# Performance work log

Hardware: AMD Instinct MI355X
Metric: run time of the kernel (lower is better)

Reference implementation:

```python
import jax, jax.numpy as jnp
import numpy as np

LN_EPS = 1e-3  # keras LayerNormalization default epsilon


def setup_inputs() -> dict:
    key = jax.random.key(0)
    ks = jax.random.split(key, 6)
    B, H, W, C = 8, 64, 64, 256
    s = 1.0 / np.sqrt(C)
    return {
        "x": jax.random.normal(ks[0], (B, H, W, C), jnp.float32),
        "gamma": jnp.ones((C,), jnp.float32),
        "beta": jnp.zeros((C,), jnp.float32),
        "wq": jax.random.normal(ks[1], (C, C), jnp.float32) * s,
        "bq": jnp.zeros((C,), jnp.float32),
        "wk": jax.random.normal(ks[2], (C, C), jnp.float32) * s,
        "bk": jnp.zeros((C,), jnp.float32),
        "wv": jax.random.normal(ks[3], (C, C), jnp.float32) * s,
        "bv": jnp.zeros((C,), jnp.float32),
        "wo": jax.random.normal(ks[4], (C, C), jnp.float32) * s,
        "bo": jnp.zeros((C,), jnp.float32),
    }


def reference(x, gamma, beta, wq, bq, wk, bk, wv, bv, wo, bo):
    B, H, W, C = x.shape
    # LayerNormalization over channel axis (keras default axis=-1, eps=1e-3)
    mean = jnp.mean(x, axis=-1, keepdims=True)
    var = jnp.mean(jnp.square(x - mean), axis=-1, keepdims=True)
    h = (x - mean) * jax.lax.rsqrt(var + LN_EPS) * gamma + beta

    q = h @ wq + bq
    k = h @ wk + bk
    v = h @ wv + bv

    # flatten spatial dims: single-head attention over N = H*W positions
    N = H * W
    qf = q.reshape(B, N, C)
    kf = k.reshape(B, N, C)
    vf = v.reshape(B, N, C)

    scale = jnp.asarray(C, x.dtype) ** -0.5
    scores = jnp.einsum('bnc,bmc->bnm', qf, kf) * scale  # [B, N, N]
    attn = jax.nn.softmax(scores, axis=-1)
    o = jnp.einsum('bnm,bmc->bnc', attn, vf).reshape(B, H, W, C)

    o = o @ wo + bo
    return x + o
```

## Files before the change

kernel.cpp:

```cpp
#include <hip/hip_runtime.h>
#include <hip/hip_bf16.h>
#include <stdint.h>

typedef __attribute__((ext_vector_type(8))) short bf16x8;
typedef __attribute__((ext_vector_type(4))) short s16x4;
typedef __attribute__((ext_vector_type(4))) float f32x4;

__device__ __forceinline__ unsigned short f2b(float x) {
  __hip_bfloat16 h = __float2bfloat16(x);
  unsigned short u;
  __builtin_memcpy(&u, &h, 2);
  return u;
}

__device__ __forceinline__ float b2f(unsigned short u) {
  unsigned v = (unsigned)u << 16;
  float f;
  __builtin_memcpy(&f, &v, 4);
  return f;
}

__device__ __forceinline__ void glds16(const void* g, void* l) {
  __builtin_amdgcn_global_load_lds((const __attribute__((address_space(1))) void*)g,
                                   (__attribute__((address_space(3))) void*)l,
                                   16, 0, 0);
}

__global__ __launch_bounds__(256) void gemm_qkv(
    const unsigned short* __restrict__ h, const unsigned short* __restrict__ wT,
    const float* __restrict__ bq, const float* __restrict__ bk, const float* __restrict__ bv,
    unsigned short* __restrict__ q, unsigned short* __restrict__ kk,
    unsigned short* __restrict__ vT, float qscale)
{
  __shared__ unsigned short As[128 * 32];
  __shared__ unsigned short Bs[128 * 32];
  const int t = threadIdx.x;
  const int lane = t & 63;
  const int wv_ = t >> 6;
  const int wr = wv_ >> 1, wc = wv_ & 1;
  const int z = blockIdx.z;
  const long long row0 = (long long)blockIdx.y * 128;
  const int col0 = blockIdx.x * 128;
  const unsigned short* Bt = wT + z * 65536;
  const float* bias = z == 0 ? bq : z == 1 ? bk : bv;
  const float scale = z == 0 ? qscale : 1.0f;

  const int sr = t >> 2;
  const int sc = (t & 3) * 8;
  const unsigned short* ga = h + (row0 + sr) * 256 + sc;
  const unsigned short* gb = Bt + (col0 + sr) * 256 + sc;
  char* lA = (char*)As + (t >> 6) * 1024;
  char* lB = (char*)Bs + (t >> 6) * 1024;

  const int l15 = lane & 15;
  const int l4 = lane >> 4;
  const unsigned short* pa = As + (wr * 64 + l15) * 32 + l4 * 8;
  const unsigned short* pb = Bs + (wc * 64 + l15) * 32 + l4 * 8;

  f32x4 acc[4][4] = {};

  for (int k0 = 0; k0 < 256; k0 += 32) {
    glds16(ga, lA);
    glds16(ga + 64 * 256, lA + 4096);
    glds16(gb, lB);
    glds16(gb + 64 * 256, lB + 4096);
    ga += 32;
    gb += 32;
    __syncthreads();
    bf16x8 a[4], b[4];
#pragma unroll
    for (int i = 0; i < 4; i++) a[i] = *(const bf16x8*)(pa + i * 512);
#pragma unroll
    for (int j = 0; j < 4; j++) b[j] = *(const bf16x8*)(pb + j * 512);
#pragma unroll
    for (int i = 0; i < 4; i++)
#pragma unroll
      for (int j = 0; j < 4; j++)
        acc[i][j] = __builtin_amdgcn_mfma_f32_16x16x32_bf16(a[i], b[j], acc[i][j], 0, 0, 0);
    __syncthreads();
  }

#pragma unroll
  for (int i = 0; i < 4; i++) {
#pragma unroll
    for (int j = 0; j < 4; j++) {
      const int col = col0 + wc * 64 + j * 16 + l15;
      const float bv_ = bias[col];
#pragma unroll
      for (int r = 0; r < 4; r++) {
        const long long row = row0 + wr * 64 + i * 16 + l4 * 4 + r;
        const float val = (acc[i][j][r] + bv_) * scale;
        if (z == 0) {
          q[row * 256 + col] = f2b(val);
        } else if (z == 1) {
          kk[row * 256 + col] = f2b(val);
        } else {
          const int bb = (int)(row >> 12), rr = (int)(row & 4095);
          const int kl = rr & 31;
          const int rrp = (rr & ~31) | ((((kl >> 2) & 3) << 3) | (((kl >> 4) & 1) << 2) | (kl & 3));
          vT[((long long)bb * 256 + col) * 4096 + rrp] = f2b(val);
        }
      }
    }
  }
}

__global__ __launch_bounds__(256) void gemm_out(
    const unsigned short* __restrict__ o0, const unsigned short* __restrict__ o1,
    const float2* __restrict__ ml0, const float2* __restrict__ ml1,
    const unsigned short* __restrict__ Bt,
    float* __restrict__ C, const float* __restrict__ bias,
    const float* __restrict__ resid)
{
  __shared__ unsigned short As[128 * 32];
  __shared__ unsigned short Bs[128 * 32];
  const int t = threadIdx.x;
  const int lane = t & 63;
  const int wv_ = t >> 6;
  const int wr = wv_ >> 1, wc = wv_ & 1;
  const long long row0 = (long long)blockIdx.y * 128;
  const int col0 = blockIdx.x * 128;

  const int sr = t >> 2;
  const int sc = (t & 3) * 8;
  const long long ar0 = row0 + sr;
  float f0a, f1a, f0b, f1b;
  {
    const float2 a = ml0[ar0], c = ml1[ar0];
    const float M = fmaxf(a.x, c.x);
    const float w0 = exp2f(a.x - M), w1 = exp2f(c.x - M);
    const float inv = 1.f / (w0 * a.y + w1 * c.y);
    f0a = w0 * inv;
    f1a = w1 * inv;
  }
  {
    const float2 a = ml0[ar0 + 64], c = ml1[ar0 + 64];
    const float M = fmaxf(a.x, c.x);
    const float w0 = exp2f(a.x - M), w1 = exp2f(c.x - M);
    const float inv = 1.f / (w0 * a.y + w1 * c.y);
    f0b = w0 * inv;
    f1b = w1 * inv;
  }
  const unsigned short* g0 = o0 + ar0 * 256 + sc;
  const unsigned short* g1 = o1 + ar0 * 256 + sc;
  const unsigned short* gb = Bt + (col0 + sr) * 256 + sc;
  char* lB = (char*)Bs + (t >> 6) * 1024;

  const int l15 = lane & 15;
  const int l4 = lane >> 4;
  const unsigned short* pa = As + (wr * 64 + l15) * 32 + l4 * 8;
  const unsigned short* pb = Bs + (wc * 64 + l15) * 32 + l4 * 8;

  f32x4 acc[4][4] = {};

  for (int k0 = 0; k0 < 256; k0 += 32) {
    bf16x8 u0 = *(const bf16x8*)g0;
    bf16x8 u1 = *(const bf16x8*)g1;
    bf16x8 v0 = *(const bf16x8*)(g0 + 64 * 256);
    bf16x8 v1 = *(const bf16x8*)(g1 + 64 * 256);
    bf16x8 m0, m1;
#pragma unroll
    for (int e = 0; e < 8; e++) {
      m0[e] = (short)f2b(f0a * b2f((unsigned short)u0[e]) + f1a * b2f((unsigned short)u1[e]));
      m1[e] = (short)f2b(f0b * b2f((unsigned short)v0[e]) + f1b * b2f((unsigned short)v1[e]));
    }
    *(bf16x8*)((char*)As + t * 16) = m0;
    *(bf16x8*)((char*)As + 4096 + t * 16) = m1;
    glds16(gb, lB);
    glds16(gb + 64 * 256, lB + 4096);
    g0 += 32;
    g1 += 32;
    gb += 32;
    __syncthreads();
    bf16x8 a[4], b[4];
#pragma unroll
    for (int i = 0; i < 4; i++) a[i] = *(const bf16x8*)(pa + i * 512);
#pragma unroll
    for (int j = 0; j < 4; j++) b[j] = *(const bf16x8*)(pb + j * 512);
#pragma unroll
    for (int i = 0; i < 4; i++)
#pragma unroll
      for (int j = 0; j < 4; j++)
        acc[i][j] = __builtin_amdgcn_mfma_f32_16x16x32_bf16(a[i], b[j], acc[i][j], 0, 0, 0);
    __syncthreads();
  }

#pragma unroll
  for (int i = 0; i < 4; i++) {
#pragma unroll
    for (int j = 0; j < 4; j++) {
      const int col = col0 + wc * 64 + j * 16 + l15;
      const float bv_ = bias[col];
#pragma unroll
      for (int r = 0; r < 4; r++) {
        const long long row = row0 + wr * 64 + i * 16 + l4 * 4 + r;
        const long long idx = row * 256 + col;
        C[idx] = resid[idx] + acc[i][j][r] + bv_;
      }
    }
  }
}

__global__ __launch_bounds__(512) void ln_bf16(const float* __restrict__ x,
                                               const float* __restrict__ gamma,
                                               const float* __restrict__ beta,
                                               unsigned short* __restrict__ h)
{
  const int w = threadIdx.x >> 6;
  const int lane = threadIdx.x & 63;
  const long long row = (long long)blockIdx.x * 8 + w;
  const f32x4 v = *(const f32x4*)(x + row * 256 + lane * 4);
  const f32x4 g = *(const f32x4*)(gamma + lane * 4);
  const f32x4 be = *(const f32x4*)(beta + lane * 4);
  float s = v[0] + v[1] + v[2] + v[3];
  float s2 = v[0] * v[0] + v[1] * v[1] + v[2] * v[2] + v[3] * v[3];
#pragma unroll
  for (int o = 32; o >= 1; o >>= 1) {
    s += __shfl_xor(s, o, 64);
    s2 += __shfl_xor(s2, o, 64);
  }
  const float mean = s * (1.f / 256.f);
  const float var = s2 * (1.f / 256.f) - mean * mean;
  const float rstd = rsqrtf(var + 1e-3f);
  s16x4 out;
#pragma unroll
  for (int e = 0; e < 4; e++) out[e] = (short)f2b((v[e] - mean) * rstd * g[e] + be[e]);
  *(s16x4*)(h + row * 256 + lane * 4) = out;
}

__global__ void wtrans(const float* __restrict__ wq, const float* __restrict__ wk,
                       const float* __restrict__ wv, const float* __restrict__ wo,
                       unsigned short* __restrict__ wT)
{
  const float* w = blockIdx.z == 0 ? wq : blockIdx.z == 1 ? wk : blockIdx.z == 2 ? wv : wo;
  unsigned short* o = wT + (long long)blockIdx.z * 65536;
  __shared__ float tile[16][17];
  const int tx = threadIdx.x, ty = threadIdx.y;
  const int bx = blockIdx.x * 16, by = blockIdx.y * 16;
  tile[ty][tx] = w[(by + ty) * 256 + bx + tx];
  __syncthreads();
  o[(bx + ty) * 256 + (by + tx)] = f2b(tile[tx][ty]);
}

#define FL_LDS (64 * 1024)

__global__ __launch_bounds__(256, 2) void flash(
    const unsigned short* __restrict__ q,
    const unsigned short* __restrict__ kk,
    const unsigned short* __restrict__ vT,
    unsigned short* __restrict__ o0,
    unsigned short* __restrict__ o1,
    float2* __restrict__ ml0,
    float2* __restrict__ ml1)
{
  extern __shared__ char lds[];
  const int t = threadIdx.x;
  const int w = t >> 6;
  const int lane = t & 63;
  const int l15 = lane & 15, hi = lane >> 4;
  const int b = blockIdx.x & 7;
  const int kh = (blockIdx.x >> 3) & 1;
  const int qb = blockIdx.x >> 4;
  const long long qrow = (long long)b * 4096 + (long long)qb * 128 + w * 32;

  const unsigned short* kbase = kk + (long long)b * 4096 * 256 + (long long)kh * 2048 * 256;
  const unsigned short* vbase = vT + (long long)b * 256 * 4096 + kh * 2048;

  const int gs_k = (t & 31) ^ ((t >> 5) & 7);
  const unsigned short* Kst = kbase + (t >> 5) * 256 + gs_k * 8;
  const int gs_v = (t & 3) ^ ((t >> 2) & 3);
  const unsigned short* Vst = vbase + (long long)(t >> 2) * 4096 + gs_v * 8;

  bf16x8 Qf[2][8];
#pragma unroll
  for (int qg = 0; qg < 2; qg++) {
    const unsigned short* qp = q + (qrow + qg * 16 + l15) * 256 + hi * 8;
#pragma unroll
    for (int ks = 0; ks < 8; ks++) Qf[qg][ks] = *(const bf16x8*)(qp + ks * 32);
  }

  f32x4 O[2][16] = {};
  float mrow[2] = {-1e30f, -1e30f};
  float lrow[2] = {0.f, 0.f};

  auto stage = [&](int it, int c) {
    const unsigned short* ks_ = Kst + (long long)it * 32 * 256;
    const unsigned short* vs_ = Vst + it * 32;
    char* kd = lds + c * 16384 + w * 1024;
    char* vd = lds + 32768 + c * 16384 + w * 1024;
#pragma unroll
    for (int p = 0; p < 4; p++) {
      glds16(ks_ + p * 8 * 256, kd + p * 4096);
      glds16(vs_ + (long long)p * 64 * 4096, vd + p * 4096);
    }
  };

  stage(0, 0);

  for (int it = 0; it < 64; ++it) {
    const int cur = it & 1;
    __builtin_amdgcn_s_barrier();
    if (it < 63) {
      stage(it + 1, cur ^ 1);
      asm volatile("s_waitcnt vmcnt(8)" ::: "memory");
    } else {
      asm volatile("s_waitcnt vmcnt(0)" ::: "memory");
    }
    __builtin_amdgcn_sched_barrier(0);
    __builtin_amdgcn_s_barrier();
    const char* Kb = lds + cur * 16384;
    const char* Vb = lds + 32768 + cur * 16384;

    f32x4 S[2][2] = {};
    __builtin_amdgcn_s_setprio(1);
#pragma unroll
    for (int ks = 0; ks < 8; ks++) {
#pragma unroll
      for (int j = 0; j < 2; j++) {
        bf16x8 Kf = *(const bf16x8*)(Kb + (j * 16 + l15) * 512 +
                                     ((ks * 64 + hi * 16) ^ ((l15 & 7) << 4)));
        S[0][j] = __builtin_amdgcn_mfma_f32_16x16x32_bf16(Kf, Qf[0][ks], S[0][j], 0, 0, 0);
        S[1][j] = __builtin_amdgcn_mfma_f32_16x16x32_bf16(Kf, Qf[1][ks], S[1][j], 0, 0, 0);
      }
    }
    __builtin_amdgcn_s_setprio(0);

    bf16x8 Pf8[2];
#pragma unroll
    for (int qg = 0; qg < 2; qg++) {
      const float mxl =
          fmaxf(fmaxf(fmaxf(S[qg][0][0], S[qg][0][1]), fmaxf(S[qg][0][2], S[qg][0][3])),
                fmaxf(fmaxf(S[qg][1][0], S[qg][1][1]), fmaxf(S[qg][1][2], S[qg][1][3])));
      if (!__all(mxl <= mrow[qg] + 8.f)) {
        float mx = fmaxf(mxl, __shfl_xor(mxl, 16, 64));
        mx = fmaxf(mx, __shfl_xor(mx, 32, 64));
        const float mn = fmaxf(mrow[qg], mx);
        const float rs_ = exp2f(mrow[qg] - mn);
        mrow[qg] = mn;
        lrow[qg] *= rs_;
#pragma unroll
        for (int dg = 0; dg < 16; dg++) O[qg][dg] *= rs_;
      }
      float sum = 0.f;
      float e[2][4];
#pragma unroll
      for (int j = 0; j < 2; j++)
#pragma unroll
        for (int r = 0; r < 4; r++) {
          e[j][r] = exp2f(S[qg][j][r] - mrow[qg]);
          sum += e[j][r];
        }
      lrow[qg] += sum;
      bf16x8 p;
#pragma unroll
      for (int j = 0; j < 2; j++)
#pragma unroll
        for (int r = 0; r < 4; r++) p[j * 4 + r] = (short)f2b(e[j][r]);
      Pf8[qg] = p;
    }

    __builtin_amdgcn_s_setprio(1);
#pragma unroll
    for (int dg = 0; dg < 16; dg++) {
      bf16x8 Vf8 = *(const bf16x8*)(Vb + (dg * 16 + l15) * 64 +
                                    ((hi * 16) ^ ((l15 & 3) << 4)));
      O[0][dg] = __builtin_amdgcn_mfma_f32_16x16x32_bf16(Vf8, Pf8[0], O[0][dg], 0, 0, 0);
      O[1][dg] = __builtin_amdgcn_mfma_f32_16x16x32_bf16(Vf8, Pf8[1], O[1][dg], 0, 0, 0);
    }
    __builtin_amdgcn_s_setprio(0);
  }

  unsigned short* const op = kh ? o1 : o0;
  float2* const mlp = kh ? ml1 : ml0;
  __syncthreads();
  char* const slab = lds + w * 16384;
#pragma unroll
  for (int qg = 0; qg < 2; qg++) {
    float lr = lrow[qg];
    lr += __shfl_xor(lr, 16, 64);
    lr += __shfl_xor(lr, 32, 64);
#pragma unroll
    for (int dg = 0; dg < 16; dg++) {
      f32x4 v = O[qg][dg];
      *(f32x4*)(slab + l15 * 1024 + ((dg * 64 + hi * 16) ^ ((l15 & 7) << 4))) = v;
    }
    if (hi == 0) mlp[qrow + qg * 16 + l15] = make_float2(mrow[qg], lr);
    const int qq = lane >> 2;
    const int dc = lane & 3;
    const long long orow = (qrow + qg * 16 + qq) * 256 + dc * 64;
#pragma unroll
    for (int half = 0; half < 8; half++) {
      bf16x8 pack;
#pragma unroll
      for (int di = 0; di < 2; di++) {
        f32x4 v = *(const f32x4*)(slab + qq * 1024 +
                                  ((dc * 256 + half * 32 + di * 16) ^ ((qq & 7) << 4)));
#pragma unroll
        for (int e2 = 0; e2 < 4; e2++) pack[di * 4 + e2] = (short)f2b(v[e2]);
      }
      *(bf16x8*)(op + orow + half * 8) = pack;
    }
    __syncthreads();
  }
}

extern "C" void kernel_launch(void* const* d_in, const int* in_sizes, int n_in,
                              void* d_out, int out_size, void* d_ws, size_t ws_size,
                              hipStream_t stream)
{
  const float* x = (const float*)d_in[0];
  const float* gamma = (const float*)d_in[1];
  const float* beta = (const float*)d_in[2];
  const float* wq = (const float*)d_in[3];
  const float* bq = (const float*)d_in[4];
  const float* wk = (const float*)d_in[5];
  const float* bk = (const float*)d_in[6];
  const float* wv = (const float*)d_in[7];
  const float* bv = (const float*)d_in[8];
  const float* wo = (const float*)d_in[9];
  const float* bo = (const float*)d_in[10];

  const int Cc = 256;
  const long long MR = 32768;

  char* base = (char*)d_ws;
  size_t off = 0;
  auto take = [&](size_t bytes) -> char* {
    char* p = base + off;
    off = (off + bytes + 255) & ~(size_t)255;
    return p;
  };
  unsigned short* h   = (unsigned short*)take((size_t)MR * Cc * 2);
  unsigned short* q   = (unsigned short*)take((size_t)MR * Cc * 2);
  unsigned short* kk  = (unsigned short*)take((size_t)MR * Cc * 2);
  unsigned short* vT  = (unsigned short*)take((size_t)MR * Cc * 2);
  unsigned short* o0  = (unsigned short*)take((size_t)MR * Cc * 2);
  unsigned short* o1  = (unsigned short*)take((size_t)MR * Cc * 2);
  unsigned short* wT  = (unsigned short*)take(4ull * Cc * Cc * 2);
  float2* ml0 = (float2*)take((size_t)MR * sizeof(float2));
  float2* ml1 = (float2*)take((size_t)MR * sizeof(float2));

  wtrans<<<dim3(16, 16, 4), dim3(16, 16), 0, stream>>>(wq, wk, wv, wo, wT);
  ln_bf16<<<dim3((unsigned)(MR / 8)), dim3(512), 0, stream>>>(x, gamma, beta, h);

  const float qscale = 0.0625f * 1.44269504f;
  gemm_qkv<<<dim3(2, 256, 3), 256, 0, stream>>>(h, wT, bq, bk, bv, q, kk, vT, qscale);

  flash<<<dim3(512), dim3(256), FL_LDS, stream>>>(q, kk, vT, o0, o1, ml0, ml1);

  gemm_out<<<dim3(2, 256, 1), 256, 0, stream>>>(o0, o1, ml0, ml1, wT + 3 * 65536,
                                                (float*)d_out, bo, x);
}
```

Measured before the change: 228.4 us.

## Split flash attention keys three ways and single-buffer K to raise occupancy

```diff
diff --git a/kernel.cpp b/kernel.cpp
--- a/kernel.cpp
+++ b/kernel.cpp
@@ -107,7 +107,9 @@
 
 __global__ __launch_bounds__(256) void gemm_out(
     const unsigned short* __restrict__ o0, const unsigned short* __restrict__ o1,
+    const unsigned short* __restrict__ o2,
     const float2* __restrict__ ml0, const float2* __restrict__ ml1,
+    const float2* __restrict__ ml2,
     const unsigned short* __restrict__ Bt,
     float* __restrict__ C, const float* __restrict__ bias,
     const float* __restrict__ resid)
@@ -124,25 +126,21 @@
   const int sr = t >> 2;
   const int sc = (t & 3) * 8;
   const long long ar0 = row0 + sr;
-  float f0a, f1a, f0b, f1b;
-  {
-    const float2 a = ml0[ar0], c = ml1[ar0];
-    const float M = fmaxf(a.x, c.x);
-    const float w0 = exp2f(a.x - M), w1 = exp2f(c.x - M);
-    const float inv = 1.f / (w0 * a.y + w1 * c.y);
-    f0a = w0 * inv;
-    f1a = w1 * inv;
-  }
-  {
-    const float2 a = ml0[ar0 + 64], c = ml1[ar0 + 64];
-    const float M = fmaxf(a.x, c.x);
-    const float w0 = exp2f(a.x - M), w1 = exp2f(c.x - M);
-    const float inv = 1.f / (w0 * a.y + w1 * c.y);
-    f0b = w0 * inv;
-    f1b = w1 * inv;
+  float fA[2][3];
+#pragma unroll
+  for (int rr = 0; rr < 2; rr++) {
+    const long long row = ar0 + rr * 64;
+    const float2 a = ml0[row], c = ml1[row], d = ml2[row];
+    const float M = fmaxf(fmaxf(a.x, c.x), d.x);
+    const float w0 = exp2f(a.x - M), w1 = exp2f(c.x - M), w2 = exp2f(d.x - M);
+    const float inv = 1.f / (w0 * a.y + w1 * c.y + w2 * d.y);
+    fA[rr][0] = w0 * inv;
+    fA[rr][1] = w1 * inv;
+    fA[rr][2] = w2 * inv;
   }
   const unsigned short* g0 = o0 + ar0 * 256 + sc;
   const unsigned short* g1 = o1 + ar0 * 256 + sc;
+  const unsigned short* g2 = o2 + ar0 * 256 + sc;
   const unsigned short* gb = Bt + (col0 + sr) * 256 + sc;
   char* lB = (char*)Bs + (t >> 6) * 1024;
 
@@ -154,22 +152,24 @@
   f32x4 acc[4][4] = {};
 
   for (int k0 = 0; k0 < 256; k0 += 32) {
-    bf16x8 u0 = *(const bf16x8*)g0;
-    bf16x8 u1 = *(const bf16x8*)g1;
-    bf16x8 v0 = *(const bf16x8*)(g0 + 64 * 256);
-    bf16x8 v1 = *(const bf16x8*)(g1 + 64 * 256);
-    bf16x8 m0, m1;
-#pragma unroll
-    for (int e = 0; e < 8; e++) {
-      m0[e] = (short)f2b(f0a * b2f((unsigned short)u0[e]) + f1a * b2f((unsigned short)u1[e]));
-      m1[e] = (short)f2b(f0b * b2f((unsigned short)v0[e]) + f1b * b2f((unsigned short)v1[e]));
-    }
-    *(bf16x8*)((char*)As + t * 16) = m0;
-    *(bf16x8*)((char*)As + 4096 + t * 16) = m1;
+#pragma unroll
+    for (int rr = 0; rr < 2; rr++) {
+      bf16x8 u0 = *(const bf16x8*)(g0 + rr * 64 * 256);
+      bf16x8 u1 = *(const bf16x8*)(g1 + rr * 64 * 256);
+      bf16x8 u2 = *(const bf16x8*)(g2 + rr * 64 * 256);
+      bf16x8 m_;
+#pragma unroll
+      for (int e = 0; e < 8; e++)
+        m_[e] = (short)f2b(fA[rr][0] * b2f((unsigned short)u0[e]) +
+                           fA[rr][1] * b2f((unsigned short)u1[e]) +
+                           fA[rr][2] * b2f((unsigned short)u2[e]));
+      *(bf16x8*)((char*)As + rr * 4096 + t * 16) = m_;
+    }
     glds16(gb, lB);
     glds16(gb + 64 * 256, lB + 4096);
     g0 += 32;
     g1 += 32;
+    g2 += 32;
     gb += 32;
     __syncthreads();
     bf16x8 a[4], b[4];
@@ -242,16 +242,15 @@
   o[(bx + ty) * 256 + (by + tx)] = f2b(tile[tx][ty]);
 }
 
-#define FL_LDS (64 * 1024)
-
-__global__ __launch_bounds__(256, 2) void flash(
+#define FL_LDS (48 * 1024)
+
+__global__ __launch_bounds__(256, 3) void flash(
     const unsigned short* __restrict__ q,
     const unsigned short* __restrict__ kk,
     const unsigned short* __restrict__ vT,
-    unsigned short* __restrict__ o0,
-    unsigned short* __restrict__ o1,
-    float2* __restrict__ ml0,
-    float2* __restrict__ ml1)
+    unsigned short* __restrict__ o0, unsigned short* __restrict__ o1,
+    unsigned short* __restrict__ o2,
+    float2* __restrict__ ml0, float2* __restrict__ ml1, float2* __restrict__ ml2)
 {
   extern __shared__ char lds[];
   const int t = threadIdx.x;
@@ -259,12 +258,15 @@
   const int lane = t & 63;
   const int l15 = lane & 15, hi = lane >> 4;
   const int b = blockIdx.x & 7;
-  const int kh = (blockIdx.x >> 3) & 1;
-  const int qb = blockIdx.x >> 4;
+  const int rem = blockIdx.x >> 3;
+  const int kh = rem % 3;
+  const int qb = rem / 3;
+  const int nit = (kh == 2) ? 42 : 43;
+  const int kbeg = kh * 1376;
   const long long qrow = (long long)b * 4096 + (long long)qb * 128 + w * 32;
 
-  const unsigned short* kbase = kk + (long long)b * 4096 * 256 + (long long)kh * 2048 * 256;
-  const unsigned short* vbase = vT + (long long)b * 256 * 4096 + kh * 2048;
+  const unsigned short* kbase = kk + (long long)b * 4096 * 256 + (long long)kbeg * 256;
+  const unsigned short* vbase = vT + (long long)b * 256 * 4096 + kbeg;
 
   const int gs_k = (t & 31) ^ ((t >> 5) & 7);
   const unsigned short* Kst = kbase + (t >> 5) * 256 + gs_k * 8;
@@ -283,33 +285,29 @@
   float mrow[2] = {-1e30f, -1e30f};
   float lrow[2] = {0.f, 0.f};
 
-  auto stage = [&](int it, int c) {
+  auto stageK = [&](int it) {
     const unsigned short* ks_ = Kst + (long long)it * 32 * 256;
+    char* kd = lds + w * 1024;
+#pragma unroll
+    for (int p = 0; p < 4; p++) glds16(ks_ + p * 8 * 256, kd + p * 4096);
+  };
+  auto stageV = [&](int it, int c) {
     const unsigned short* vs_ = Vst + it * 32;
-    char* kd = lds + c * 16384 + w * 1024;
-    char* vd = lds + 32768 + c * 16384 + w * 1024;
-#pragma unroll
-    for (int p = 0; p < 4; p++) {
-      glds16(ks_ + p * 8 * 256, kd + p * 4096);
-      glds16(vs_ + (long long)p * 64 * 4096, vd + p * 4096);
-    }
+    char* vd = lds + 16384 + c * 16384 + w * 1024;
+#pragma unroll
+    for (int p = 0; p < 4; p++) glds16(vs_ + (long long)p * 64 * 4096, vd + p * 4096);
   };
 
-  stage(0, 0);
-
-  for (int it = 0; it < 64; ++it) {
+  stageK(0);
+  stageV(0, 0);
+
+  for (int it = 0; it < nit; ++it) {
     const int cur = it & 1;
-    __builtin_amdgcn_s_barrier();
-    if (it < 63) {
-      stage(it + 1, cur ^ 1);
-      asm volatile("s_waitcnt vmcnt(8)" ::: "memory");
-    } else {
-      asm volatile("s_waitcnt vmcnt(0)" ::: "memory");
-    }
+    asm volatile("s_waitcnt vmcnt(0)" ::: "memory");
     __builtin_amdgcn_sched_barrier(0);
     __builtin_amdgcn_s_barrier();
-    const char* Kb = lds + cur * 16384;
-    const char* Vb = lds + 32768 + cur * 16384;
+    const char* Kb = lds;
+    const char* Vb = lds + 16384 + cur * 16384;
 
     f32x4 S[2][2] = {};
     __builtin_amdgcn_s_setprio(1);
@@ -324,6 +322,12 @@
       }
     }
     __builtin_amdgcn_s_setprio(0);
+    __builtin_amdgcn_sched_barrier(0);
+    __builtin_amdgcn_s_barrier();
+    if (it < nit - 1) {
+      stageK(it + 1);
+      stageV(it + 1, cur ^ 1);
+    }
 
     bf16x8 Pf8[2];
 #pragma unroll
@@ -370,10 +374,10 @@
     __builtin_amdgcn_s_setprio(0);
   }
 
-  unsigned short* const op = kh ? o1 : o0;
-  float2* const mlp = kh ? ml1 : ml0;
+  unsigned short* const op = kh == 0 ? o0 : kh == 1 ? o1 : o2;
+  float2* const mlp = kh == 0 ? ml0 : kh == 1 ? ml1 : ml2;
   __syncthreads();
-  char* const slab = lds + w * 16384;
+  char* const slab = lds + w * 8192;
 #pragma unroll
   for (int qg = 0; qg < 2; qg++) {
     float lr = lrow[qg];
@@ -381,24 +385,20 @@
     lr += __shfl_xor(lr, 32, 64);
 #pragma unroll
     for (int dg = 0; dg < 16; dg++) {
-      f32x4 v = O[qg][dg];
-      *(f32x4*)(slab + l15 * 1024 + ((dg * 64 + hi * 16) ^ ((l15 & 7) << 4))) = v;
+      s16x4 pk;
+#pragma unroll
+      for (int r = 0; r < 4; r++) pk[r] = (short)f2b(O[qg][dg][r]);
+      *(s16x4*)(slab + l15 * 512 + ((dg * 32 + hi * 8) ^ ((l15 & 7) << 4))) = pk;
     }
     if (hi == 0) mlp[qrow + qg * 16 + l15] = make_float2(mrow[qg], lr);
     const int qq = lane >> 2;
     const int dc = lane & 3;
     const long long orow = (qrow + qg * 16 + qq) * 256 + dc * 64;
 #pragma unroll
-    for (int half = 0; half < 8; half++) {
-      bf16x8 pack;
-#pragma unroll
-      for (int di = 0; di < 2; di++) {
-        f32x4 v = *(const f32x4*)(slab + qq * 1024 +
-                                  ((dc * 256 + half * 32 + di * 16) ^ ((qq & 7) << 4)));
-#pragma unroll
-        for (int e2 = 0; e2 < 4; e2++) pack[di * 4 + e2] = (short)f2b(v[e2]);
-      }
-      *(bf16x8*)(op + orow + half * 8) = pack;
+    for (int st = 0; st < 8; st++) {
+      bf16x8 v = *(const bf16x8*)(slab + qq * 512 +
+                                  ((dc * 128 + st * 16) ^ ((qq & 7) << 4)));
+      *(bf16x8*)(op + orow + st * 8) = v;
     }
     __syncthreads();
   }
@@ -436,9 +436,11 @@
   unsigned short* vT  = (unsigned short*)take((size_t)MR * Cc * 2);
   unsigned short* o0  = (unsigned short*)take((size_t)MR * Cc * 2);
   unsigned short* o1  = (unsigned short*)take((size_t)MR * Cc * 2);
+  unsigned short* o2  = h;
   unsigned short* wT  = (unsigned short*)take(4ull * Cc * Cc * 2);
   float2* ml0 = (float2*)take((size_t)MR * sizeof(float2));
   float2* ml1 = (float2*)take((size_t)MR * sizeof(float2));
+  float2* ml2 = (float2*)take((size_t)MR * sizeof(float2));
 
   wtrans<<<dim3(16, 16, 4), dim3(16, 16), 0, stream>>>(wq, wk, wv, wo, wT);
   ln_bf16<<<dim3((unsigned)(MR / 8)), dim3(512), 0, stream>>>(x, gamma, beta, h);
@@ -446,8 +448,8 @@
   const float qscale = 0.0625f * 1.44269504f;
   gemm_qkv<<<dim3(2, 256, 3), 256, 0, stream>>>(h, wT, bq, bk, bv, q, kk, vT, qscale);
 
-  flash<<<dim3(512), dim3(256), FL_LDS, stream>>>(q, kk, vT, o0, o1, ml0, ml1);
-
-  gemm_out<<<dim3(2, 256, 1), 256, 0, stream>>>(o0, o1, ml0, ml1, wT + 3 * 65536,
-                                                (float*)d_out, bo, x);
-}
+  flash<<<dim3(768), dim3(256), FL_LDS, stream>>>(q, kk, vT, o0, o1, o2, ml0, ml1, ml2);
+
+  gemm_out<<<dim3(2, 256, 1), 256, 0, stream>>>(o0, o1, o2, ml0, ml1, ml2,
+                                                wT + 3 * 65536, (float*)d_out, bo, x);
+}
```

New measurement: 529.6 us. +131.9%, slower.

## Fuse LayerNorm into QKV projection with LDS-resident normalized tile

Applied to the files above, without the earlier changes.

```diff
diff --git a/kernel.cpp b/kernel.cpp
--- a/kernel.cpp
+++ b/kernel.cpp
@@ -26,79 +26,110 @@
                                    16, 0, 0);
 }
 
-__global__ __launch_bounds__(256) void gemm_qkv(
-    const unsigned short* __restrict__ h, const unsigned short* __restrict__ wT,
-    const float* __restrict__ bq, const float* __restrict__ bk, const float* __restrict__ bv,
+#define LQ_LDS (80 * 1024)
+
+__global__ __launch_bounds__(256, 2) void ln_qkv(
+    const float* __restrict__ x, const float* __restrict__ gamma,
+    const float* __restrict__ beta, const unsigned short* __restrict__ wT,
+    const float* __restrict__ bq, const float* __restrict__ bk,
+    const float* __restrict__ bv,
     unsigned short* __restrict__ q, unsigned short* __restrict__ kk,
     unsigned short* __restrict__ vT, float qscale)
 {
-  __shared__ unsigned short As[128 * 32];
-  __shared__ unsigned short Bs[128 * 32];
+  extern __shared__ char lds[];
   const int t = threadIdx.x;
   const int lane = t & 63;
-  const int wv_ = t >> 6;
-  const int wr = wv_ >> 1, wc = wv_ & 1;
-  const int z = blockIdx.z;
+  const int w = t >> 6;
+  const int wr = w >> 1, wc = w & 1;
   const long long row0 = (long long)blockIdx.y * 128;
   const int col0 = blockIdx.x * 128;
-  const unsigned short* Bt = wT + z * 65536;
-  const float* bias = z == 0 ? bq : z == 1 ? bk : bv;
-  const float scale = z == 0 ? qscale : 1.0f;
 
   const int sr = t >> 2;
   const int sc = (t & 3) * 8;
-  const unsigned short* ga = h + (row0 + sr) * 256 + sc;
-  const unsigned short* gb = Bt + (col0 + sr) * 256 + sc;
-  char* lA = (char*)As + (t >> 6) * 1024;
-  char* lB = (char*)Bs + (t >> 6) * 1024;
+
+  auto stageB = [&](int st, int c) {
+    const unsigned short* gb = wT + (st >> 3) * 65536 +
+                               (long long)(col0 + sr) * 256 + (st & 7) * 32 + sc;
+    char* d = lds + 65536 + c * 8192 + w * 1024;
+    glds16(gb, d);
+    glds16(gb + 64 * 256, d + 4096);
+  };
+
+  stageB(0, 0);
+
+  {
+    const f32x4 g4 = *(const f32x4*)(gamma + lane * 4);
+    const f32x4 b4 = *(const f32x4*)(beta + lane * 4);
+    for (int rr = 0; rr < 32; rr++) {
+      const int rl = w * 32 + rr;
+      const f32x4 v = *(const f32x4*)(x + (row0 + rl) * 256 + lane * 4);
+      float s = v[0] + v[1] + v[2] + v[3];
+      float s2 = v[0] * v[0] + v[1] * v[1] + v[2] * v[2] + v[3] * v[3];
+#pragma unroll
+      for (int o = 32; o >= 1; o >>= 1) {
+        s += __shfl_xor(s, o, 64);
+        s2 += __shfl_xor(s2, o, 64);
+      }
+      const float mean = s * (1.f / 256.f);
+      const float var = s2 * (1.f / 256.f) - mean * mean;
+      const float rstd = rsqrtf(var + 1e-3f);
+      s16x4 hv;
+#pragma unroll
+      for (int e = 0; e < 4; e++) hv[e] = (short)f2b((v[e] - mean) * rstd * g4[e] + b4[e]);
+      *(s16x4*)(lds + ((rl * 512 + lane * 8) ^ ((rl & 7) << 4))) = hv;
+    }
+  }
 
   const int l15 = lane & 15;
   const int l4 = lane >> 4;
-  const unsigned short* pa = As + (wr * 64 + l15) * 32 + l4 * 8;
-  const unsigned short* pb = Bs + (wc * 64 + l15) * 32 + l4 * 8;
-
-  f32x4 acc[4][4] = {};
-
-  for (int k0 = 0; k0 < 256; k0 += 32) {
-    glds16(ga, lA);
-    glds16(ga + 64 * 256, lA + 4096);
-    glds16(gb, lB);
-    glds16(gb + 64 * 256, lB + 4096);
-    ga += 32;
-    gb += 32;
-    __syncthreads();
-    bf16x8 a[4], b[4];
-#pragma unroll
-    for (int i = 0; i < 4; i++) a[i] = *(const bf16x8*)(pa + i * 512);
-#pragma unroll
-    for (int j = 0; j < 4; j++) b[j] = *(const bf16x8*)(pb + j * 512);
-#pragma unroll
-    for (int i = 0; i < 4; i++)
+  int step = 0;
+#pragma unroll
+  for (int z = 0; z < 3; z++) {
+    f32x4 acc[4][4] = {};
+#pragma unroll
+    for (int k0 = 0; k0 < 8; k0++, step++) {
+      const int cur = step & 1;
+      __syncthreads();
+      if (step < 23) stageB(step + 1, cur ^ 1);
+      bf16x8 a[4], b[4];
+#pragma unroll
+      for (int i = 0; i < 4; i++) {
+        const int row = wr * 64 + i * 16 + l15;
+        a[i] = *(const bf16x8*)(lds + ((row * 512 + k0 * 64 + l4 * 16) ^ ((l15 & 7) << 4)));
+      }
+      const char* pb = lds + 65536 + cur * 8192;
 #pragma unroll
       for (int j = 0; j < 4; j++)
-        acc[i][j] = __builtin_amdgcn_mfma_f32_16x16x32_bf16(a[i], b[j], acc[i][j], 0, 0, 0);
-    __syncthreads();
-  }
-
-#pragma unroll
-  for (int i = 0; i < 4; i++) {
-#pragma unroll
-    for (int j = 0; j < 4; j++) {
-      const int col = col0 + wc * 64 + j * 16 + l15;
-      const float bv_ = bias[col];
-#pragma unroll
-      for (int r = 0; r < 4; r++) {
-        const long long row = row0 + wr * 64 + i * 16 + l4 * 4 + r;
-        const float val = (acc[i][j][r] + bv_) * scale;
-        if (z == 0) {
-          q[row * 256 + col] = f2b(val);
-        } else if (z == 1) {
-          kk[row * 256 + col] = f2b(val);
-        } else {
-          const int bb = (int)(row >> 12), rr = (int)(row & 4095);
-          const int kl = rr & 31;
-          const int rrp = (rr & ~31) | ((((kl >> 2) & 3) << 3) | (((kl >> 4) & 1) << 2) | (kl & 3));
-          vT[((long long)bb * 256 + col) * 4096 + rrp] = f2b(val);
+        b[j] = *(const bf16x8*)(pb + (wc * 64 + j * 16 + l15) * 64 + l4 * 16);
+#pragma unroll
+      for (int i = 0; i < 4; i++)
+#pragma unroll
+        for (int j = 0; j < 4; j++)
+          acc[i][j] = __builtin_amdgcn_mfma_f32_16x16x32_bf16(a[i], b[j], acc[i][j], 0, 0, 0);
+    }
+    const float* bias = z == 0 ? bq : z == 1 ? bk : bv;
+    const float scale = z == 0 ? qscale : 1.0f;
+#pragma unroll
+    for (int i = 0; i < 4; i++) {
+#pragma unroll
+      for (int j = 0; j < 4; j++) {
+        const int col = col0 + wc * 64 + j * 16 + l15;
+        const float bv_ = bias[col];
+#pragma unroll
+        for (int r = 0; r < 4; r++) {
+          const long long row = row0 + wr * 64 + i * 16 + l4 * 4 + r;
+          const float val = (acc[i][j][r] + bv_) * scale;
+          if (z == 0) {
+            q[row * 256 + col] = f2b(val);
+          } else if (z == 1) {
+            kk[row * 256 + col] = f2b(val);
+          } else {
+            const int bb = (int)(row >> 12), rr = (int)(row & 4095);
+            const int kl = rr & 31;
+            const int rrp = (rr & ~31) |
+                            ((((kl >> 2) & 3) << 3) | (((kl >> 4) & 1) << 2) | (kl & 3));
+            vT[((long long)bb * 256 + col) * 4096 + rrp] = f2b(val);
+          }
         }
       }
     }
@@ -199,33 +230,6 @@
       }
     }
   }
-}
-
-__global__ __launch_bounds__(512) void ln_bf16(const float* __restrict__ x,
-                                               const float* __restrict__ gamma,
-                                               const float* __restrict__ beta,
-                                               unsigned short* __restrict__ h)
-{
-  const int w = threadIdx.x >> 6;
-  const int lane = threadIdx.x & 63;
-  const long long row = (long long)blockIdx.x * 8 + w;
-  const f32x4 v = *(const f32x4*)(x + row * 256 + lane * 4);
-  const f32x4 g = *(const f32x4*)(gamma + lane * 4);
-  const f32x4 be = *(const f32x4*)(beta + lane * 4);
-  float s = v[0] + v[1] + v[2] + v[3];
-  float s2 = v[0] * v[0] + v[1] * v[1] + v[2] * v[2] + v[3] * v[3];
-#pragma unroll
-  for (int o = 32; o >= 1; o >>= 1) {
-    s += __shfl_xor(s, o, 64);
-    s2 += __shfl_xor(s2, o, 64);
-  }
-  const float mean = s * (1.f / 256.f);
-  const float var = s2 * (1.f / 256.f) - mean * mean;
-  const float rstd = rsqrtf(var + 1e-3f);
-  s16x4 out;
-#pragma unroll
-  for (int e = 0; e < 4; e++) out[e] = (short)f2b((v[e] - mean) * rstd * g[e] + be[e]);
-  *(s16x4*)(h + row * 256 + lane * 4) = out;
 }
 
 __global__ void wtrans(const float* __restrict__ wq, const float* __restrict__ wk,
@@ -430,7 +434,6 @@
     off = (off + bytes + 255) & ~(size_t)255;
     return p;
   };
-  unsigned short* h   = (unsigned short*)take((size_t)MR * Cc * 2);
   unsigned short* q   = (unsigned short*)take((size_t)MR * Cc * 2);
   unsigned short* kk  = (unsigned short*)take((size_t)MR * Cc * 2);
   unsigned short* vT  = (unsigned short*)take((size_t)MR * Cc * 2);
@@ -441,10 +444,10 @@
   float2* ml1 = (float2*)take((size_t)MR * sizeof(float2));
 
   wtrans<<<dim3(16, 16, 4), dim3(16, 16), 0, stream>>>(wq, wk, wv, wo, wT);
-  ln_bf16<<<dim3((unsigned)(MR / 8)), dim3(512), 0, stream>>>(x, gamma, beta, h);
 
   const float qscale = 0.0625f * 1.44269504f;
-  gemm_qkv<<<dim3(2, 256, 3), 256, 0, stream>>>(h, wT, bq, bk, bv, q, kk, vT, qscale);
+  ln_qkv<<<dim3(2, 256), dim3(256), LQ_LDS, stream>>>(x, gamma, beta, wT, bq, bk, bv,
+                                                      q, kk, vT, qscale);
 
   flash<<<dim3(512), dim3(256), FL_LDS, stream>>>(q, kk, vT, o0, o1, ml0, ml1);
 
```

Result: faster. 219.5 us, median of 2 (-3.9%).
